# Optimization experiments

Measured on AMD Instinct MI355X. Metric: run time of the kernel, lower is better.

## Reference

```python
import jax, jax.numpy as jnp
import numpy as np
from jax import lax

H, W = 26, 26          # largest feature-map size for resnet18(2,3) @ 224 after AvgPool2d(3,1)
D = 384                # 128 + 256 concatenated channels
M = 200000             # coreset memory-bank size
IMG = 224
K = 5
SIGMA = 4.0
KS = 2 * int(4.0 * SIGMA + 0.5) + 1  # 33, torchvision-style gaussian blur kernel


def _l2_normalize(x, eps=1e-12):
    n = jnp.linalg.norm(x, axis=-1, keepdims=True)
    return x / jnp.maximum(n, eps)


def _gaussian_kernel1d():
    r = (KS - 1) // 2
    x = jnp.arange(-r, r + 1, dtype=jnp.float32)
    k = jnp.exp(-0.5 * (x / SIGMA) ** 2)
    return k / jnp.sum(k)


def _gaussian_blur(x):
    # x: [1,1,IMG,IMG]; separable gaussian with reflect padding
    k = _gaussian_kernel1d()
    r = (KS - 1) // 2
    x = jnp.pad(x, ((0, 0), (0, 0), (r, r), (r, r)), mode='reflect')
    kh = k.reshape(1, 1, KS, 1)
    kw = k.reshape(1, 1, 1, KS)
    x = lax.conv_general_dilated(x, kh, (1, 1), 'VALID')
    x = lax.conv_general_dilated(x, kw, (1, 1), 'VALID')
    return x


def setup_inputs() -> dict:
    key = jax.random.key(0)
    k1, k2 = jax.random.split(key)
    patch = jax.random.normal(k1, (H * W, D), dtype=jnp.float32)
    patch_lib = _l2_normalize(jax.random.normal(k2, (M, D), dtype=jnp.float32))
    return {"patch": patch, "patch_lib": patch_lib}


def reference(patch, patch_lib):
    # patch: [N, D] raw concatenated features; patch_lib: [M, D] (pre-normalized at fit time)
    patch = _l2_normalize(patch)  # F.normalize(patch, p=2, dim=1)

    # torch.cdist(patch, patch_lib) via ||a||^2 + ||b||^2 - 2 a.b
    pn = jnp.sum(patch * patch, axis=1, keepdims=True)      # [N,1]
    ln = jnp.sum(patch_lib * patch_lib, axis=1)             # [M]
    d2 = pn + ln[None, :] - 2.0 * (patch @ patch_lib.T)     # [N,M]
    dist = jnp.sqrt(jnp.maximum(d2, 0.0))

    min_val = jnp.min(dist, axis=1)                         # [N]
    min_idx = jnp.argmin(dist, axis=1)                      # [N]
    s_idx = jnp.argmax(min_val)
    s_star = min_val[s_idx]

    m_test_star = patch[s_idx]                              # [D]
    m_star = patch_lib[min_idx[s_idx]]                      # [D]

    # cdist(m_star, patch_lib) + topk(k=5, largest=False)
    d_star2 = ln + jnp.sum(m_star * m_star) - 2.0 * (patch_lib @ m_star)  # [M]
    d_star = jnp.sqrt(jnp.maximum(d_star2, 0.0))
    _, nn_idx = lax.top_k(-d_star, K)
    nb_vectors = patch_lib[nn_idx]                          # [K, D]
    nb_dists = jnp.linalg.norm(m_test_star[None, :] - nb_vectors, axis=1)

    numerator = jnp.exp(jnp.linalg.norm(m_test_star - m_star))
    denominator = jnp.sum(jnp.exp(nb_dists))
    w = 1.0 - numerator / denominator
    s = w * s_star

    s_map = min_val.reshape(1, 1, H, W)
    # F.interpolate bilinear, align_corners=False == half-pixel linear resize
    s_map = jax.image.resize(s_map, (1, 1, IMG, IMG), method='linear')
    s_map = _gaussian_blur(s_map)
    return s, s_map
```

## Files before the change

### kernel.cpp

```cpp
#include <hip/hip_runtime.h>
#include <stdint.h>

#define NP    676
#define NPAD  768
#define DD    384
#define MM    200000
#define IMG   224

typedef unsigned int u32;
typedef unsigned long long u64;
typedef short bf16x8 __attribute__((ext_vector_type(8)));
typedef float f32x4 __attribute__((ext_vector_type(4)));

#define WS_PACKED   0u
#define WS_SCAL     6144u
#define WS_MV       6400u
#define WS_TOPS     9728u
#define WS_PNORM    15360u
#define WS_PNB      1195008u
#define WS_DSTAR    1784832u
#define WS_BUFA     3384832u
#define WS_BUFB     3585536u
#define WS_LIBH     3786240u

__device__ inline unsigned short f2bf(float f) {
  u32 u = __float_as_uint(f);
  u += 0x7FFFu + ((u >> 16) & 1u);
  return (unsigned short)(u >> 16);
}
__device__ inline float bflo(u32 u) { return __uint_as_float(u << 16); }
__device__ inline float bfhi(u32 u) { return __uint_as_float(u & 0xFFFF0000u); }

__device__ __forceinline__ void gld16(const void* g, void* l) {
  __builtin_amdgcn_global_load_lds((const __attribute__((address_space(1))) u32*)g,
                                   (__attribute__((address_space(3))) u32*)l, 16, 0, 0);
}

__global__ void k_norm(const float* __restrict__ patch, float* __restrict__ pnorm,
                       unsigned short* __restrict__ pnb, u64* __restrict__ packed_) {
  __shared__ float red[2];
  __shared__ float scs;
  int i = blockIdx.x, t = threadIdx.x;
  if (i < 6) packed_[i * 128 + t] = 0ull;
  if (i >= NP) {
    for (int j = 0; j < 3; ++j) {
      pnorm[(size_t)i * DD + t + 128 * j] = 0.f;
      pnb[(size_t)i * DD + t + 128 * j] = 0;
    }
    return;
  }
  float x0 = patch[(size_t)i * DD + t];
  float x1 = patch[(size_t)i * DD + t + 128];
  float x2 = patch[(size_t)i * DD + t + 256];
  float s = x0 * x0 + x1 * x1 + x2 * x2;
#pragma unroll
  for (int m = 1; m < 64; m <<= 1) s += __shfl_xor(s, m, 64);
  if ((t & 63) == 0) red[t >> 6] = s;
  __syncthreads();
  if (t == 0) scs = 1.f / fmaxf(sqrtf(red[0] + red[1]), 1e-12f);
  __syncthreads();
  float k = scs;
  pnorm[(size_t)i * DD + t]       = x0 * k;
  pnorm[(size_t)i * DD + t + 128] = x1 * k;
  pnorm[(size_t)i * DD + t + 256] = x2 * k;
  pnb[(size_t)i * DD + t]       = f2bf(x0 * k);
  pnb[(size_t)i * DD + t + 128] = f2bf(x1 * k);
  pnb[(size_t)i * DD + t + 256] = f2bf(x2 * k);
}

__global__ void k_conv(const float* __restrict__ lib, unsigned short* __restrict__ libh) {
  const size_t n4 = (size_t)MM * DD / 8;
  const size_t stride = (size_t)gridDim.x * 256;
  const float4* src = (const float4*)lib;
  uint4* dst = (uint4*)libh;
  for (size_t i = (size_t)blockIdx.x * 256 + threadIdx.x; i < n4; i += stride) {
    float4 f0 = src[2 * i], f1 = src[2 * i + 1];
    uint4 o;
    o.x = (u32)f2bf(f0.x) | ((u32)f2bf(f0.y) << 16);
    o.y = (u32)f2bf(f0.z) | ((u32)f2bf(f0.w) << 16);
    o.z = (u32)f2bf(f1.x) | ((u32)f2bf(f1.y) << 16);
    o.w = (u32)f2bf(f1.z) | ((u32)f2bf(f1.w) << 16);
    dst[i] = o;
  }
}

__global__ __launch_bounds__(256, 2) void k_pass1(const unsigned short* __restrict__ pnb,
                                                  const unsigned short* __restrict__ libh,
                                                  u64* __restrict__ packed_) {
  __shared__ __align__(16) unsigned short bt[4 * 6144];
  const int t = threadIdx.x;
  const int xcd = blockIdx.x & 7;
  const int idx = blockIdx.x >> 3;
  const int logical = (xcd < 4 ? xcd * 587 : 4 * 587 + (xcd - 4) * 586) + idx;
  const int cc = logical / 6, rg = logical - cc * 6;
  const int col0 = cc * 256;
  const int rowbase = rg * 128;
  const int wave = t >> 6, lane = t & 63;
  const int quad = lane >> 4, l15 = lane & 15;
  const int nchunk = (MM - col0 < 256) ? (MM - col0) / 16 : 16;

  u32 soff[3];
#pragma unroll
  for (int it = 0; it < 3; ++it) {
    int slot = (wave * 3 + it) * 64 + lane;
    int r = slot / 48, u = slot - r * 48;
    soff[it] = (u32)(r * 768 + ((u ^ (r & 7)) << 4));
  }
  int bo[12];
#pragma unroll
  for (int kt = 0; kt < 12; ++kt)
    bo[kt] = l15 * 768 + (((quad + kt * 4) ^ (l15 & 7)) << 4);

  bf16x8 areg[2][12];
#pragma unroll
  for (int q = 0; q < 2; ++q) {
    if (q) __syncthreads();
#pragma unroll
    for (int j = 0; j < 4; ++j) {
      const char* srcb = (const char*)pnb + (size_t)(rowbase + (q * 4 + j) * 16) * 768;
#pragma unroll
      for (int it = 0; it < 3; ++it)
        gld16(srcb + soff[it], (char*)bt + j * 12288 + (wave * 3 + it) * 1024);
    }
    __syncthreads();
    if ((wave >> 1) == q) {
#pragma unroll
      for (int mi = 0; mi < 2; ++mi)
#pragma unroll
        for (int kt = 0; kt < 12; ++kt)
          areg[mi][kt] = *(const bf16x8*)((const char*)bt +
                                          ((wave & 1) * 2 + mi) * 12288 + bo[kt]);
    }
  }
  __syncthreads();

  u32 best[8];
#pragma unroll
  for (int j = 0; j < 8; ++j) best[j] = 0u;

  const char* bsrc = (const char*)libh + (size_t)col0 * 768;
#pragma unroll
  for (int pc = 0; pc < 3; ++pc) {
#pragma unroll
    for (int it = 0; it < 3; ++it)
      gld16(bsrc + (size_t)pc * 12288 + soff[it],
            (char*)bt + pc * 12288 + (wave * 3 + it) * 1024);
  }

#pragma unroll 1
  for (int c = 0; c < nchunk; ++c) {
    if (c + 3 <= nchunk)      asm volatile("s_waitcnt vmcnt(6)" ::: "memory");
    else if (c + 2 == nchunk) asm volatile("s_waitcnt vmcnt(3)" ::: "memory");
    else                      asm volatile("s_waitcnt vmcnt(0)" ::: "memory");
    __builtin_amdgcn_s_barrier();
    __builtin_amdgcn_sched_barrier(0);
    if (c + 3 < nchunk) {
      const int nb = (c + 3) & 3;
#pragma unroll
      for (int it = 0; it < 3; ++it)
        gld16(bsrc + (size_t)(c + 3) * 12288 + soff[it],
              (char*)bt + nb * 12288 + (wave * 3 + it) * 1024);
    }
    const char* bufb = (const char*)bt + (c & 3) * 12288;
    bf16x8 bfr[12];
#pragma unroll
    for (int kt = 0; kt < 12; ++kt) bfr[kt] = *(const bf16x8*)(bufb + bo[kt]);
    f32x4 acc[2];
#pragma unroll
    for (int mi = 0; mi < 2; ++mi) {
      acc[mi][0] = 0.f; acc[mi][1] = 0.f; acc[mi][2] = 0.f; acc[mi][3] = 0.f;
    }
#pragma unroll
    for (int kt = 0; kt < 12; ++kt) {
#pragma unroll
      for (int mi = 0; mi < 2; ++mi)
        acc[mi] = __builtin_amdgcn_mfma_f32_16x16x32_bf16(areg[mi][kt], bfr[kt], acc[mi], 0, 0, 0);
    }
    const u32 colbits = 255u - (u32)(c * 16 + l15);
#pragma unroll
    for (int mi = 0; mi < 2; ++mi)
#pragma unroll
      for (int r = 0; r < 4; ++r) {
        u32 kb = __float_as_uint(acc[mi][r] + 3.0f);
        u32 k = (kb & 0xFFFFFF00u) | colbits;
        if (k > best[mi * 4 + r]) best[mi * 4 + r] = k;
      }
  }

#pragma unroll
  for (int mi = 0; mi < 2; ++mi)
#pragma unroll
    for (int r = 0; r < 4; ++r) {
      u32 k = best[mi * 4 + r];
#pragma unroll
      for (int m = 1; m < 16; m <<= 1) {
        u32 o = (u32)__shfl_xor((int)k, m, 64);
        k = o > k ? o : k;
      }
      if (l15 == 0) {
        int col = col0 + 255 - (int)(k & 255u);
        int row = rowbase + wave * 32 + mi * 16 + quad * 4 + r;
        u64 g = ((u64)(k & 0xFFFFFF00u) << 32) | (u64)(0xFFFFFFFFu - (u32)col);
        atomicMax(&packed_[row], g);
      }
    }
}

__global__ void k_select(const u64* __restrict__ packed_, u32* __restrict__ scal,
                         float* __restrict__ mv) {
  __shared__ u64 red[256];
  int t = threadIdx.x;
  u64 best = 0ull;
  for (int i = t; i < NP; i += 256) {
    u64 p = packed_[i];
    float d = __uint_as_float((u32)(p >> 32)) - 3.0f;
    float dist = sqrtf(fmaxf(2.f - 2.f * d, 0.f));
    mv[i] = dist;
    u64 key = ((u64)__float_as_uint(dist) << 32) | (u32)(0xFFFFFFFFu - (u32)i);
    if (key > best) best = key;
  }
  red[t] = best;
  __syncthreads();
  for (int s = 128; s > 0; s >>= 1) {
    if (t < s && red[t + s] > red[t]) red[t] = red[t + s];
    __syncthreads();
  }
  if (t == 0) {
    u64 k = red[0];
    u32 sidx = 0xFFFFFFFFu - (u32)k;
    u64 p = packed_[sidx];
    u32 jstar = 0xFFFFFFFFu - (u32)p;
    scal[0] = sidx;
    scal[1] = jstar;
    ((float*)scal)[2] = __uint_as_float((u32)(k >> 32));
  }
}

__global__ void k_dstar(const unsigned short* __restrict__ libh, const u32* __restrict__ scal,
                        u64* __restrict__ dstar) {
  int gid = blockIdx.x * 256 + threadIdx.x;
  int w = gid >> 6, lane = gid & 63;
  int quad = lane >> 4, l15 = lane & 15;
  u32 jstar = scal[1];
  const uint4* ms = (const uint4*)(libh + (size_t)jstar * DD);
  float mf[24];
#pragma unroll
  for (int j = 0; j < 3; ++j) {
    uint4 u = ms[j * 16 + l15];
    mf[j * 8 + 0] = bflo(u.x); mf[j * 8 + 1] = bfhi(u.x);
    mf[j * 8 + 2] = bflo(u.y); mf[j * 8 + 3] = bfhi(u.y);
    mf[j * 8 + 4] = bflo(u.z); mf[j * 8 + 5] = bfhi(u.z);
    mf[j * 8 + 6] = bflo(u.w); mf[j * 8 + 7] = bfhi(u.w);
  }
  for (int r4 = w; r4 < 50000; r4 += 3200) {
    int row = r4 * 4 + quad;
    const uint4* xr = (const uint4*)(libh + (size_t)row * DD);
    float dot = 0.f;
#pragma unroll
    for (int j = 0; j < 3; ++j) {
      uint4 u = xr[j * 16 + l15];
      dot += mf[j * 8 + 0] * bflo(u.x) + mf[j * 8 + 1] * bfhi(u.x);
      dot += mf[j * 8 + 2] * bflo(u.y) + mf[j * 8 + 3] * bfhi(u.y);
      dot += mf[j * 8 + 4] * bflo(u.z) + mf[j * 8 + 5] * bfhi(u.z);
      dot += mf[j * 8 + 6] * bflo(u.w) + mf[j * 8 + 7] * bfhi(u.w);
    }
#pragma unroll
    for (int mm = 1; mm < 16; mm <<= 1) dot += __shfl_xor(dot, mm, 64);
    if (l15 == 0) {
      float dist = sqrtf(fmaxf(2.f - 2.f * dot, 0.f));
      dstar[row] = ((u64)__float_as_uint(dist) << 32) | (u32)row;
    }
  }
}

__device__ inline void merge5(const u64* a, const u64* b, u64* o) {
  int ia = 0, ib = 0;
#pragma unroll
  for (int j = 0; j < 5; ++j) {
    u64 va = a[ia], vb = b[ib];
    if (va <= vb) { o[j] = va; ++ia; } else { o[j] = vb; ++ib; }
  }
}

__global__ void k_top5a(const u64* __restrict__ dstar, u64* __restrict__ tops) {
  __shared__ u64 l[256 * 5];
  int t = threadIdx.x, b = blockIdx.x;
  int start = b * 1563;
  int end = start + 1563; if (end > MM) end = MM;
  u64 a0 = ~0ull, a1 = ~0ull, a2 = ~0ull, a3 = ~0ull, a4 = ~0ull;
  for (int i = start + t; i < end; i += 256) {
    u64 v = dstar[i];
    if (v < a4) {
      if (v < a0)      { a4 = a3; a3 = a2; a2 = a1; a1 = a0; a0 = v; }
      else if (v < a1) { a4 = a3; a3 = a2; a2 = a1; a1 = v; }
      else if (v < a2) { a4 = a3; a3 = a2; a2 = v; }
      else if (v < a3) { a4 = a3; a3 = v; }
      else             { a4 = v; }
    }
  }
  l[t * 5 + 0] = a0; l[t * 5 + 1] = a1; l[t * 5 + 2] = a2; l[t * 5 + 3] = a3; l[t * 5 + 4] = a4;
  __syncthreads();
  for (int s = 128; s > 0; s >>= 1) {
    if (t < s) {
      u64 o[5];
      merge5(&l[t * 5], &l[(t + s) * 5], o);
#pragma unroll
      for (int j = 0; j < 5; ++j) l[t * 5 + j] = o[j];
    }
    __syncthreads();
  }
  if (t < 5) tops[b * 5 + t] = l[t];
}

__global__ void k_final(const u64* __restrict__ tops, const u32* __restrict__ scal,
                        const float* __restrict__ pnorm, const float* __restrict__ lib,
                        float* __restrict__ out) {
  __shared__ u64 l[128 * 5];
  __shared__ u32 nn[5];
  int t = threadIdx.x;
  if (t < 128) {
#pragma unroll
    for (int j = 0; j < 5; ++j) l[t * 5 + j] = tops[t * 5 + j];
  }
  __syncthreads();
  for (int s = 64; s > 0; s >>= 1) {
    if (t < s) {
      u64 o[5];
      merge5(&l[t * 5], &l[(t + s) * 5], o);
#pragma unroll
      for (int j = 0; j < 5; ++j) l[t * 5 + j] = o[j];
    }
    __syncthreads();
  }
  if (t < 5) nn[t] = (u32)l[t];
  __syncthreads();
  if (t < 64) {
    int lane = t;
    u32 sidx = scal[0], jstar = scal[1];
    const float* mt = pnorm + (size_t)sidx * DD;
    float mtv[6];
#pragma unroll
    for (int r = 0; r < 6; ++r) mtv[r] = mt[lane + 64 * r];
    float dist[6];
    for (int n = 0; n < 6; ++n) {
      u32 idx = (n == 0) ? jstar : nn[n - 1];
      const float* v = lib + (size_t)idx * DD;
      float p = 0.f;
#pragma unroll
      for (int r = 0; r < 6; ++r) {
        float d = mtv[r] - v[lane + 64 * r];
        p += d * d;
      }
#pragma unroll
      for (int m = 1; m < 64; m <<= 1) p += __shfl_xor(p, m, 64);
      dist[n] = sqrtf(p);
    }
    if (lane == 0) {
      float nrm = dist[0];
      float den = 0.f;
      for (int n = 1; n < 6; ++n) den += expf(dist[n]);
      out[0] = (1.f - expf(nrm) / den) * nrm;
    }
  }
}

__global__ void k_resize(const float* __restrict__ mv, float* __restrict__ A) {
  int i = blockIdx.x * 256 + threadIdx.x;
  int Y = i / IMG, X = i - Y * IMG;
  const float sc = 26.f / 224.f;
  float sy = (Y + 0.5f) * sc - 0.5f;
  float sx = (X + 0.5f) * sc - 0.5f;
  float fy = sy - floorf(sy), fx = sx - floorf(sx);
  int y0 = (int)floorf(sy), x0 = (int)floorf(sx);
  int y1 = y0 + 1, x1 = x0 + 1;
  y0 = min(max(y0, 0), 25); y1 = min(max(y1, 0), 25);
  x0 = min(max(x0, 0), 25); x1 = min(max(x1, 0), 25);
  float v00 = mv[y0 * 26 + x0], v01 = mv[y0 * 26 + x1];
  float v10 = mv[y1 * 26 + x0], v11 = mv[y1 * 26 + x1];
  A[i] = (1.f - fy) * ((1.f - fx) * v00 + fx * v01) + fy * ((1.f - fx) * v10 + fx * v11);
}

__global__ void k_blurh(const float* __restrict__ A, float* __restrict__ B) {
  __shared__ float kw[33];
  __shared__ float kinv;
  int t = threadIdx.x;
  if (t < 33) {
    float x = ((float)t - 16.f) * 0.25f;
    kw[t] = expf(-0.5f * x * x);
  }
  __syncthreads();
  if (t == 0) {
    float s = 0.f;
    for (int j = 0; j < 33; ++j) s += kw[j];
    kinv = 1.f / s;
  }
  __syncthreads();
  int i = blockIdx.x * 256 + t;
  int Y = i / IMG, X = i - Y * IMG;
  float s = 0.f;
  for (int j = 0; j < 33; ++j) {
    int xx = X + j - 16;
    xx = xx < 0 ? -xx : (xx > 223 ? 446 - xx : xx);
    s += kw[j] * A[Y * IMG + xx];
  }
  B[i] = s * kinv;
}

__global__ void k_blurv(const float* __restrict__ B, float* __restrict__ out) {
  __shared__ float kw[33];
  __shared__ float kinv;
  int t = threadIdx.x;
  if (t < 33) {
    float x = ((float)t - 16.f) * 0.25f;
    kw[t] = expf(-0.5f * x * x);
  }
  __syncthreads();
  if (t == 0) {
    float s = 0.f;
    for (int j = 0; j < 33; ++j) s += kw[j];
    kinv = 1.f / s;
  }
  __syncthreads();
  int i = blockIdx.x * 256 + t;
  int Y = i / IMG, X = i - Y * IMG;
  float s = 0.f;
  for (int j = 0; j < 33; ++j) {
    int yy = Y + j - 16;
    yy = yy < 0 ? -yy : (yy > 223 ? 446 - yy : yy);
    s += kw[j] * B[yy * IMG + X];
  }
  out[1 + i] = s * kinv;
}

extern "C" void kernel_launch(void* const* d_in, const int* in_sizes, int n_in,
                              void* d_out, int out_size, void* d_ws, size_t ws_size,
                              hipStream_t stream) {
  const float* patch = (const float*)d_in[0];
  const float* lib   = (const float*)d_in[1];
  float* out = (float*)d_out;
  char* w = (char*)d_ws;

  u64*  packed_ = (u64*)(w + WS_PACKED);
  u32*  scal    = (u32*)(w + WS_SCAL);
  float* mv     = (float*)(w + WS_MV);
  u64*  tops    = (u64*)(w + WS_TOPS);
  float* pnorm  = (float*)(w + WS_PNORM);
  unsigned short* pnb  = (unsigned short*)(w + WS_PNB);
  u64*  dstar   = (u64*)(w + WS_DSTAR);
  float* bufA   = (float*)(w + WS_BUFA);
  float* bufB   = (float*)(w + WS_BUFB);
  unsigned short* libh = (unsigned short*)(w + WS_LIBH);

  k_norm  <<<NPAD, 128, 0, stream>>>(patch, pnorm, pnb, packed_);
  k_conv  <<<2048, 256, 0, stream>>>(lib, libh);
  k_pass1 <<<4692, 256, 0, stream>>>(pnb, libh, packed_);
  k_select<<<1,    256, 0, stream>>>(packed_, scal, mv);
  k_dstar <<<800,  256, 0, stream>>>(libh, scal, dstar);
  k_top5a <<<128,  256, 0, stream>>>(dstar, tops);
  k_final <<<1,    256, 0, stream>>>(tops, scal, pnorm, lib, out);
  k_resize<<<196,  256, 0, stream>>>(mv, bufA);
  k_blurh <<<196,  256, 0, stream>>>(bufA, bufB);
  k_blurv <<<196,  256, 0, stream>>>(bufB, out);
}
```

Measured before the change: 604.7 us.

## Fuse bf16 conversion of memory bank into pass1 and read fp32 in dstar

Removes the separate k_conv kernel that wrote a bf16 copy of the 200000x384 library. k_pass1 now loads fp32 library tiles into registers, converts them with v_cvt_pk_bf16_f32 and stores them into a swizzled double-buffered LDS, with register prefetch two chunks ahead. k_dstar reads fp32 rows directly. This saves one full write and read pass of the bf16 copy, but pass1 now reads twice as many bytes per chunk (fp32) and loses the async global-to-LDS path and the deeper 4-stage pipeline.

```diff
diff --git a/kernel.cpp b/kernel.cpp
--- a/kernel.cpp
+++ b/kernel.cpp
@@ -21,15 +21,18 @@
 #define WS_DSTAR    1784832u
 #define WS_BUFA     3384832u
 #define WS_BUFB     3585536u
-#define WS_LIBH     3786240u
 
 __device__ inline unsigned short f2bf(float f) {
   u32 u = __float_as_uint(f);
   u += 0x7FFFu + ((u >> 16) & 1u);
   return (unsigned short)(u >> 16);
 }
-__device__ inline float bflo(u32 u) { return __uint_as_float(u << 16); }
-__device__ inline float bfhi(u32 u) { return __uint_as_float(u & 0xFFFF0000u); }
+
+__device__ __forceinline__ u32 cvtpk(float lo, float hi) {
+  u32 r;
+  asm("v_cvt_pk_bf16_f32 %0, %1, %2" : "=v"(r) : "v"(lo), "v"(hi));
+  return r;
+}
 
 __device__ __forceinline__ void gld16(const void* g, void* l) {
   __builtin_amdgcn_global_load_lds((const __attribute__((address_space(1))) u32*)g,
@@ -68,26 +71,10 @@
   pnb[(size_t)i * DD + t + 256] = f2bf(x2 * k);
 }
 
-__global__ void k_conv(const float* __restrict__ lib, unsigned short* __restrict__ libh) {
-  const size_t n4 = (size_t)MM * DD / 8;
-  const size_t stride = (size_t)gridDim.x * 256;
-  const float4* src = (const float4*)lib;
-  uint4* dst = (uint4*)libh;
-  for (size_t i = (size_t)blockIdx.x * 256 + threadIdx.x; i < n4; i += stride) {
-    float4 f0 = src[2 * i], f1 = src[2 * i + 1];
-    uint4 o;
-    o.x = (u32)f2bf(f0.x) | ((u32)f2bf(f0.y) << 16);
-    o.y = (u32)f2bf(f0.z) | ((u32)f2bf(f0.w) << 16);
-    o.z = (u32)f2bf(f1.x) | ((u32)f2bf(f1.y) << 16);
-    o.w = (u32)f2bf(f1.z) | ((u32)f2bf(f1.w) << 16);
-    dst[i] = o;
-  }
-}
-
 __global__ __launch_bounds__(256, 2) void k_pass1(const unsigned short* __restrict__ pnb,
-                                                  const unsigned short* __restrict__ libh,
+                                                  const float* __restrict__ lib,
                                                   u64* __restrict__ packed_) {
-  __shared__ __align__(16) unsigned short bt[4 * 6144];
+  __shared__ __align__(16) unsigned short bt[2 * 6144];
   const int t = threadIdx.x;
   const int xcd = blockIdx.x & 7;
   const int idx = blockIdx.x >> 3;
@@ -99,37 +86,45 @@
   const int quad = lane >> 4, l15 = lane & 15;
   const int nchunk = (MM - col0 < 256) ? (MM - col0) / 16 : 16;
 
-  u32 soff[3];
+  u32 srcoff[3], wdst[3];
 #pragma unroll
   for (int it = 0; it < 3; ++it) {
-    int slot = (wave * 3 + it) * 64 + lane;
-    int r = slot / 48, u = slot - r * 48;
-    soff[it] = (u32)(r * 768 + ((u ^ (r & 7)) << 4));
+    int s = it * 256 + t;
+    int r = s / 48, u = s - r * 48;
+    srcoff[it] = (u32)(r * 1536 + u * 32);
+    wdst[it]   = (u32)(r * 768 + ((u ^ (r & 7)) << 4));
   }
   int bo[12];
 #pragma unroll
   for (int kt = 0; kt < 12; ++kt)
-    bo[kt] = l15 * 768 + (((quad + kt * 4) ^ (l15 & 7)) << 4);
+    bo[kt] = l15 * 768 + (((quad + 4 * kt) ^ (l15 & 7)) << 4);
 
   bf16x8 areg[2][12];
-#pragma unroll
-  for (int q = 0; q < 2; ++q) {
-    if (q) __syncthreads();
-#pragma unroll
-    for (int j = 0; j < 4; ++j) {
-      const char* srcb = (const char*)pnb + (size_t)(rowbase + (q * 4 + j) * 16) * 768;
-#pragma unroll
-      for (int it = 0; it < 3; ++it)
-        gld16(srcb + soff[it], (char*)bt + j * 12288 + (wave * 3 + it) * 1024);
-    }
-    __syncthreads();
-    if ((wave >> 1) == q) {
-#pragma unroll
-      for (int mi = 0; mi < 2; ++mi)
-#pragma unroll
-        for (int kt = 0; kt < 12; ++kt)
-          areg[mi][kt] = *(const bf16x8*)((const char*)bt +
-                                          ((wave & 1) * 2 + mi) * 12288 + bo[kt]);
+  {
+    u32 soffA[6];
+#pragma unroll
+    for (int it = 0; it < 6; ++it) {
+      int s = (wave * 6 + it) * 64 + lane;
+      int r = s / 48, u = s - r * 48;
+      soffA[it] = (u32)(r * 768 + ((u ^ (r & 7)) << 4));
+    }
+#pragma unroll
+    for (int q = 0; q < 4; ++q) {
+      if (q) __syncthreads();
+      const char* srcb = (const char*)pnb + (size_t)(rowbase + q * 32) * 768;
+#pragma unroll
+      for (int it = 0; it < 6; ++it)
+        gld16(srcb + soffA[it], (char*)bt + (wave * 6 + it) * 1024);
+      __syncthreads();
+      if (wave == q) {
+#pragma unroll
+        for (int mi = 0; mi < 2; ++mi)
+#pragma unroll
+          for (int kt = 0; kt < 12; ++kt)
+            areg[mi][kt] = *(const bf16x8*)((const char*)bt +
+                            (size_t)(mi * 16 + l15) * 768 +
+                            (((quad + 4 * kt) ^ (l15 & 7)) << 4));
+      }
     }
   }
   __syncthreads();
@@ -138,33 +133,58 @@
 #pragma unroll
   for (int j = 0; j < 8; ++j) best[j] = 0u;
 
-  const char* bsrc = (const char*)libh + (size_t)col0 * 768;
-#pragma unroll
-  for (int pc = 0; pc < 3; ++pc) {
-#pragma unroll
-    for (int it = 0; it < 3; ++it)
-      gld16(bsrc + (size_t)pc * 12288 + soff[it],
-            (char*)bt + pc * 12288 + (wave * 3 + it) * 1024);
-  }
-
+  const char* bsrc = (const char*)lib + (size_t)col0 * 1536;
+  float4 preg[3][2];
+
+  {
+#pragma unroll
+    for (int it = 0; it < 3; ++it) {
+      preg[it][0] = *(const float4*)(bsrc + srcoff[it]);
+      preg[it][1] = *(const float4*)(bsrc + srcoff[it] + 16);
+    }
+#pragma unroll
+    for (int it = 0; it < 3; ++it) {
+      uint4 o;
+      o.x = cvtpk(preg[it][0].x, preg[it][0].y);
+      o.y = cvtpk(preg[it][0].z, preg[it][0].w);
+      o.z = cvtpk(preg[it][1].x, preg[it][1].y);
+      o.w = cvtpk(preg[it][1].z, preg[it][1].w);
+      *(uint4*)((char*)bt + wdst[it]) = o;
+    }
+    if (nchunk > 1) {
+      const char* s1 = bsrc + 24576;
+#pragma unroll
+      for (int it = 0; it < 3; ++it) {
+        preg[it][0] = *(const float4*)(s1 + srcoff[it]);
+        preg[it][1] = *(const float4*)(s1 + srcoff[it] + 16);
+      }
+    }
+  }
+
+  int cur = 0;
 #pragma unroll 1
   for (int c = 0; c < nchunk; ++c) {
-    if (c + 3 <= nchunk)      asm volatile("s_waitcnt vmcnt(6)" ::: "memory");
-    else if (c + 2 == nchunk) asm volatile("s_waitcnt vmcnt(3)" ::: "memory");
-    else                      asm volatile("s_waitcnt vmcnt(0)" ::: "memory");
-    __builtin_amdgcn_s_barrier();
-    __builtin_amdgcn_sched_barrier(0);
-    if (c + 3 < nchunk) {
-      const int nb = (c + 3) & 3;
-#pragma unroll
-      for (int it = 0; it < 3; ++it)
-        gld16(bsrc + (size_t)(c + 3) * 12288 + soff[it],
-              (char*)bt + nb * 12288 + (wave * 3 + it) * 1024);
-    }
-    const char* bufb = (const char*)bt + (c & 3) * 12288;
-    bf16x8 bfr[12];
-#pragma unroll
-    for (int kt = 0; kt < 12; ++kt) bfr[kt] = *(const bf16x8*)(bufb + bo[kt]);
+    __syncthreads();
+    if (c + 1 < nchunk) {
+#pragma unroll
+      for (int it = 0; it < 3; ++it) {
+        uint4 o;
+        o.x = cvtpk(preg[it][0].x, preg[it][0].y);
+        o.y = cvtpk(preg[it][0].z, preg[it][0].w);
+        o.z = cvtpk(preg[it][1].x, preg[it][1].y);
+        o.w = cvtpk(preg[it][1].z, preg[it][1].w);
+        *(uint4*)((char*)bt + (cur ^ 1) * 12288 + wdst[it]) = o;
+      }
+    }
+    if (c + 2 < nchunk) {
+      const char* s2 = bsrc + (size_t)(c + 2) * 24576;
+#pragma unroll
+      for (int it = 0; it < 3; ++it) {
+        preg[it][0] = *(const float4*)(s2 + srcoff[it]);
+        preg[it][1] = *(const float4*)(s2 + srcoff[it] + 16);
+      }
+    }
+    const char* bufb = (const char*)bt + cur * 12288;
     f32x4 acc[2];
 #pragma unroll
     for (int mi = 0; mi < 2; ++mi) {
@@ -172,9 +192,10 @@
     }
 #pragma unroll
     for (int kt = 0; kt < 12; ++kt) {
+      bf16x8 bf = *(const bf16x8*)(bufb + bo[kt]);
 #pragma unroll
       for (int mi = 0; mi < 2; ++mi)
-        acc[mi] = __builtin_amdgcn_mfma_f32_16x16x32_bf16(areg[mi][kt], bfr[kt], acc[mi], 0, 0, 0);
+        acc[mi] = __builtin_amdgcn_mfma_f32_16x16x32_bf16(areg[mi][kt], bf, acc[mi], 0, 0, 0);
     }
     const u32 colbits = 255u - (u32)(c * 16 + l15);
 #pragma unroll
@@ -185,6 +206,7 @@
         u32 k = (kb & 0xFFFFFF00u) | colbits;
         if (k > best[mi * 4 + r]) best[mi * 4 + r] = k;
       }
+    cur ^= 1;
   }
 
 #pragma unroll
@@ -236,33 +258,24 @@
   }
 }
 
-__global__ void k_dstar(const unsigned short* __restrict__ libh, const u32* __restrict__ scal,
+__global__ void k_dstar(const float* __restrict__ lib, const u32* __restrict__ scal,
                         u64* __restrict__ dstar) {
   int gid = blockIdx.x * 256 + threadIdx.x;
   int w = gid >> 6, lane = gid & 63;
   int quad = lane >> 4, l15 = lane & 15;
   u32 jstar = scal[1];
-  const uint4* ms = (const uint4*)(libh + (size_t)jstar * DD);
-  float mf[24];
-#pragma unroll
-  for (int j = 0; j < 3; ++j) {
-    uint4 u = ms[j * 16 + l15];
-    mf[j * 8 + 0] = bflo(u.x); mf[j * 8 + 1] = bfhi(u.x);
-    mf[j * 8 + 2] = bflo(u.y); mf[j * 8 + 3] = bfhi(u.y);
-    mf[j * 8 + 4] = bflo(u.z); mf[j * 8 + 5] = bfhi(u.z);
-    mf[j * 8 + 6] = bflo(u.w); mf[j * 8 + 7] = bfhi(u.w);
-  }
+  const float4* ms = (const float4*)(lib + (size_t)jstar * DD);
+  float4 mf[6];
+#pragma unroll
+  for (int j = 0; j < 6; ++j) mf[j] = ms[j * 16 + l15];
   for (int r4 = w; r4 < 50000; r4 += 3200) {
     int row = r4 * 4 + quad;
-    const uint4* xr = (const uint4*)(libh + (size_t)row * DD);
+    const float4* xr = (const float4*)(lib + (size_t)row * DD);
     float dot = 0.f;
 #pragma unroll
-    for (int j = 0; j < 3; ++j) {
-      uint4 u = xr[j * 16 + l15];
-      dot += mf[j * 8 + 0] * bflo(u.x) + mf[j * 8 + 1] * bfhi(u.x);
-      dot += mf[j * 8 + 2] * bflo(u.y) + mf[j * 8 + 3] * bfhi(u.y);
-      dot += mf[j * 8 + 4] * bflo(u.z) + mf[j * 8 + 5] * bfhi(u.z);
-      dot += mf[j * 8 + 6] * bflo(u.w) + mf[j * 8 + 7] * bfhi(u.w);
+    for (int j = 0; j < 6; ++j) {
+      float4 u = xr[j * 16 + l15];
+      dot += mf[j].x * u.x + mf[j].y * u.y + mf[j].z * u.z + mf[j].w * u.w;
     }
 #pragma unroll
     for (int mm = 1; mm < 16; mm <<= 1) dot += __shfl_xor(dot, mm, 64);
@@ -449,13 +462,11 @@
   u64*  dstar   = (u64*)(w + WS_DSTAR);
   float* bufA   = (float*)(w + WS_BUFA);
   float* bufB   = (float*)(w + WS_BUFB);
-  unsigned short* libh = (unsigned short*)(w + WS_LIBH);
 
   k_norm  <<<NPAD, 128, 0, stream>>>(patch, pnorm, pnb, packed_);
-  k_conv  <<<2048, 256, 0, stream>>>(lib, libh);
-  k_pass1 <<<4692, 256, 0, stream>>>(pnb, libh, packed_);
+  k_pass1 <<<4692, 256, 0, stream>>>(pnb, lib, packed_);
   k_select<<<1,    256, 0, stream>>>(packed_, scal, mv);
-  k_dstar <<<800,  256, 0, stream>>>(libh, scal, dstar);
+  k_dstar <<<800,  256, 0, stream>>>(lib, scal, dstar);
   k_top5a <<<128,  256, 0, stream>>>(dstar, tops);
   k_final <<<1,    256, 0, stream>>>(tops, scal, pnorm, lib, out);
   k_resize<<<196,  256, 0, stream>>>(mv, bufA);
```

New measurement: 586.4 us. -3.0%, faster.
